# Performance work log

Hardware: AMD Instinct MI355X
Metric: run time of the kernel (lower is better)

Reference implementation:

```python
import jax, jax.numpy as jnp
import numpy as np

N = 50000
E = 800000
IN_DIM = 128
HID_DIM = 128
OUT_DIM = 128
EPS = 1e-5


def setup_inputs() -> dict:
    key = jax.random.key(0)
    ks = jax.random.split(key, 6)
    x = jax.random.normal(ks[0], (N, IN_DIM), dtype=jnp.float32)
    src = jax.random.randint(ks[1], (E,), 0, N, dtype=jnp.int32)
    dst = jax.random.randint(ks[2], (E,), 0, N, dtype=jnp.int32)
    W1 = jax.random.normal(ks[3], (IN_DIM, HID_DIM), dtype=jnp.float32) / np.sqrt(IN_DIM)
    W2 = jax.random.normal(ks[4], (HID_DIM, OUT_DIM), dtype=jnp.float32) / np.sqrt(HID_DIM)
    return {
        "x": x, "src": src, "dst": dst,
        "W1": W1, "b1": jnp.zeros((HID_DIM,), jnp.float32),
        "gamma1": jnp.ones((HID_DIM,), jnp.float32), "beta1": jnp.zeros((HID_DIM,), jnp.float32),
        "W2": W2, "b2": jnp.zeros((OUT_DIM,), jnp.float32),
        "gamma2": jnp.ones((OUT_DIM,), jnp.float32), "beta2": jnp.zeros((OUT_DIM,), jnp.float32),
    }


def _degrees(src, dst, n):
    ones = jnp.ones(src.shape[0], jnp.float32)
    out_deg = jax.ops.segment_sum(ones, src, num_segments=n)
    in_deg = jax.ops.segment_sum(ones, dst, num_segments=n)
    # DGL norm='both' clamps degree to min 1 before pow(-0.5)
    return jnp.clip(out_deg, 1.0) ** -0.5, jnp.clip(in_deg, 1.0) ** -0.5


def _gconv(h, src, dst, d_out, d_in, W, b):
    h = h * d_out[:, None]                                   # [N, d] src-side norm
    m = jax.ops.segment_sum(h[src], dst, num_segments=h.shape[0])  # SpMM aggregate
    m = m * d_in[:, None]                                    # dst-side norm
    return m @ W + b


def _bn(h, gamma, beta):
    mu = jnp.mean(h, axis=0)
    var = jnp.var(h, axis=0)  # biased, matches torch BN training forward
    return gamma * (h - mu) * jax.lax.rsqrt(var + EPS) + beta


def reference(x, src, dst, W1, b1, gamma1, beta1, W2, b2, gamma2, beta2):
    d_out, d_in = _degrees(src, dst, x.shape[0])
    h1 = jax.nn.relu(_bn(_gconv(x, src, dst, d_out, d_in, W1, b1), gamma1, beta1))
    # dropout is identity in eval mode
    h2 = _bn(_gconv(h1, src, dst, d_out, d_in, W2, b2), gamma2, beta2)
    return jax.nn.relu(h2 + h1)
```

## Files before the change

### kernel.cpp

```cpp
#include <hip/hip_runtime.h>
#include <hip/hip_fp16.h>

#define NODES 50000
#define EDGES 800000
#define DIM 128
#define EPS_BN 1e-5f
#define SCAN_B 1024
#define SCAN_NB ((NODES + SCAN_B - 1) / SCAN_B)
#define GEMM_NB ((NODES + 63) / 64)
#define NCH 64
#define CHE (EDGES / NCH)
#define NR 4
#define RNG (NODES / NR)

typedef _Float16 half8 __attribute__((ext_vector_type(8)));
typedef float floatx4 __attribute__((ext_vector_type(4)));

union H8 { half8 v; __half2 h2[4]; };

__global__ __launch_bounds__(256) void hist_part_kernel(const int* __restrict__ src,
                                                        const int* __restrict__ dst,
                                                        unsigned short* __restrict__ Psrc,
                                                        unsigned short* __restrict__ Pdst) {
    __shared__ int h[RNG];
    int chunk = blockIdx.x & (NCH - 1);
    int range = blockIdx.x >> 6;
    const int* arr = blockIdx.y ? dst : src;
    unsigned short* P = blockIdx.y ? Pdst : Psrc;
    int base = range * RNG;
    for (int i = threadIdx.x; i < RNG; i += 256) h[i] = 0;
    __syncthreads();
    int e0 = chunk * CHE;
    for (int e = e0 + threadIdx.x; e < e0 + CHE; e += 256) {
        unsigned r = (unsigned)(arr[e] - base);
        if (r < (unsigned)RNG) atomicAdd(&h[r], 1);
    }
    __syncthreads();
    for (int i = threadIdx.x; i < RNG; i += 256)
        P[(size_t)chunk * NODES + base + i] = (unsigned short)h[i];
}

__global__ __launch_bounds__(256) void combine_kernel(const unsigned short* __restrict__ Psrc,
                                                      unsigned short* __restrict__ Pdst,
                                                      int* __restrict__ cnt_in,
                                                      float* __restrict__ dn_out,
                                                      float* __restrict__ sdeg,
                                                      float* __restrict__ dn_in) {
    int v = blockIdx.x * 256 + threadIdx.x;
    if (v >= NODES) return;
    int s = 0;
    #pragma unroll 8
    for (int j = 0; j < NCH; ++j) s += Psrc[(size_t)j * NODES + v];
    float fs = (float)max(s, 1);
    dn_out[v] = rsqrtf(fs);
    sdeg[v] = sqrtf(fs);
    int run = 0;
    #pragma unroll 8
    for (int j = 0; j < NCH; ++j) {
        int t = Pdst[(size_t)j * NODES + v];
        Pdst[(size_t)j * NODES + v] = (unsigned short)run;
        run += t;
    }
    cnt_in[v] = run;
    dn_in[v] = rsqrtf((float)max(run, 1));
}

__global__ __launch_bounds__(SCAN_B) void scan_p1_kernel(const int* __restrict__ cnt,
                                                         int* __restrict__ row_ptr,
                                                         int* __restrict__ blk_sums) {
    __shared__ int sm[SCAN_B];
    int t = threadIdx.x;
    int idx = blockIdx.x * SCAN_B + t;
    int v = (idx < NODES) ? cnt[idx] : 0;
    sm[t] = v;
    __syncthreads();
    #pragma unroll
    for (int off = 1; off < SCAN_B; off <<= 1) {
        int u = (t >= off) ? sm[t - off] : 0;
        __syncthreads();
        sm[t] += u;
        __syncthreads();
    }
    if (idx < NODES) row_ptr[idx] = sm[t] - v;
    if (t == SCAN_B - 1) blk_sums[blockIdx.x] = sm[t];
}

__global__ __launch_bounds__(SCAN_B) void scan_p3_kernel(int* __restrict__ row_ptr,
                                                         const int* __restrict__ blk_sums) {
    __shared__ int soff;
    int t = threadIdx.x;
    if (t < 64) {
        int v = (t < blockIdx.x) ? blk_sums[t] : 0;
        #pragma unroll
        for (int off = 32; off > 0; off >>= 1) v += __shfl_xor(v, off);
        if (t == 0) soff = v;
    }
    __syncthreads();
    int idx = blockIdx.x * SCAN_B + t;
    if (idx < NODES) row_ptr[idx] += soff;
    if (idx == 0) row_ptr[NODES] = EDGES;
}

__global__ __launch_bounds__(256) void fill_kernel(const int* __restrict__ src,
                                                   const int* __restrict__ dst,
                                                   const int* __restrict__ row_ptr,
                                                   const unsigned short* __restrict__ Pdst,
                                                   int* __restrict__ csr_src) {
    __shared__ int h[RNG];
    int chunk = blockIdx.x & (NCH - 1);
    int range = blockIdx.x >> 6;
    int base = range * RNG;
    for (int i = threadIdx.x; i < RNG; i += 256) h[i] = 0;
    __syncthreads();
    int e0 = chunk * CHE;
    const unsigned short* Pj = Pdst + (size_t)chunk * NODES;
    for (int e = e0 + threadIdx.x; e < e0 + CHE; e += 256) {
        int d = dst[e];
        unsigned r = (unsigned)(d - base);
        if (r < (unsigned)RNG) {
            int local = atomicAdd(&h[r], 1);
            csr_src[row_ptr[d] + (int)Pj[d] + local] = src[e];
        }
    }
}

__global__ __launch_bounds__(256) void w2h_kernel(const float* __restrict__ W1,
                                                  const float* __restrict__ W2,
                                                  __half* __restrict__ WhT1,
                                                  __half* __restrict__ WhT2,
                                                  float* __restrict__ p2) {
    int idx = blockIdx.x * 256 + threadIdx.x;
    if (blockIdx.x < 32) p2[blockIdx.x * 256 + threadIdx.x] = 0.f;
    const float* W = (idx < 16384) ? W1 : W2;
    __half* D = (idx < 16384) ? WhT1 : WhT2;
    int i = idx & 16383;
    int n = i >> 7;
    int k = i & 127;
    D[i] = __float2half(W[k * DIM + n]);
}

__global__ __launch_bounds__(256) void prescale_kernel(const float* __restrict__ x,
                                                       const float* __restrict__ dn_out,
                                                       __half* __restrict__ hs) {
    int idx = blockIdx.x * 256 + threadIdx.x;
    if (idx >= NODES * 16) return;
    int row = idx >> 4;
    int c8 = (idx & 15) * 8;
    float sc = dn_out[row];
    const float* xp = x + (size_t)row * DIM + c8;
    float4 v0 = *(const float4*)xp;
    float4 v1 = *(const float4*)(xp + 4);
    H8 u;
    u.h2[0] = __floats2half2_rn(v0.x * sc, v0.y * sc);
    u.h2[1] = __floats2half2_rn(v0.z * sc, v0.w * sc);
    u.h2[2] = __floats2half2_rn(v1.x * sc, v1.y * sc);
    u.h2[3] = __floats2half2_rn(v1.z * sc, v1.w * sc);
    *(half8*)((char*)hs + ((size_t)row * DIM + c8) * 2) = u.v;
}

__device__ __forceinline__ void acc_h8(half8 raw, float* a) {
    H8 u; u.v = raw;
    #pragma unroll
    for (int k = 0; k < 4; ++k) {
        float2 f = __half22float2(u.h2[k]);
        a[2 * k] += f.x;
        a[2 * k + 1] += f.y;
    }
}

__global__ __launch_bounds__(256) void pull_kernel(const __half* __restrict__ hs,
                                                   const int* __restrict__ row_ptr,
                                                   const int* __restrict__ csr_src,
                                                   const float* __restrict__ dn_in,
                                                   __half* __restrict__ agg) {
    int wid = threadIdx.x >> 6;
    int node = blockIdx.x * 4 + wid;
    if (node >= NODES) return;
    int lane = threadIdx.x & 63;
    int q = lane >> 4;
    int c = lane & 15;
    const char* base = (const char*)hs;
    int beg = row_ptr[node];
    int end = row_ptr[node + 1];
    float a[8];
    #pragma unroll
    for (int i = 0; i < 8; ++i) a[i] = 0.f;
    int eb = beg;
    for (; eb + 8 <= end; eb += 8) {
        int s0 = csr_src[eb + q];
        int s1 = csr_src[eb + 4 + q];
        half8 v0 = *(const half8*)(base + (size_t)s0 * 256 + c * 16);
        half8 v1 = *(const half8*)(base + (size_t)s1 * 256 + c * 16);
        acc_h8(v0, a);
        acc_h8(v1, a);
    }
    for (; eb + 4 <= end; eb += 4) {
        int s0 = csr_src[eb + q];
        half8 v0 = *(const half8*)(base + (size_t)s0 * 256 + c * 16);
        acc_h8(v0, a);
    }
    if (eb + q < end) {
        int s0 = csr_src[eb + q];
        half8 v0 = *(const half8*)(base + (size_t)s0 * 256 + c * 16);
        acc_h8(v0, a);
    }
    #pragma unroll
    for (int i = 0; i < 8; ++i) a[i] += __shfl_xor(a[i], 32);
    #pragma unroll
    for (int i = 0; i < 8; ++i) a[i] += __shfl_xor(a[i], 16);
    if (lane < 16) {
        float sc = dn_in[node];
        H8 u;
        #pragma unroll
        for (int k = 0; k < 4; ++k)
            u.h2[k] = __floats2half2_rn(a[2 * k] * sc, a[2 * k + 1] * sc);
        *(half8*)((char*)agg + (size_t)node * 256 + c * 16) = u.v;
    }
}

__global__ __launch_bounds__(256) void gemm_mfma_kernel(const __half* __restrict__ A,
                                                        const __half* __restrict__ WhT,
                                                        const float* __restrict__ bias,
                                                        __half* __restrict__ hraw,
                                                        float* __restrict__ p2) {
    __shared__ float smem[8704];
    __half* wl = (__half*)smem;

    int t = threadIdx.x;

    #pragma unroll
    for (int i = 0; i < 8; ++i) {
        int cch = t + 256 * i;
        int n = cch >> 4;
        int ch = cch & 15;
        *(float4*)((char*)wl + n * 272 + ch * 16) =
            *(const float4*)((const char*)WhT + n * 256 + ch * 16);
    }

    int w = t >> 6;
    int lane = t & 63;
    int m = lane & 15;
    int quad = lane >> 4;
    int r0 = blockIdx.x * 64 + w * 16;
    int arow = r0 + m;

    half8 afrag[4];
    if (arow < NODES) {
        const char* ap = (const char*)(A + (size_t)arow * DIM);
        #pragma unroll
        for (int kt = 0; kt < 4; ++kt)
            afrag[kt] = *(const half8*)(ap + kt * 64 + quad * 16);
    } else {
        #pragma unroll
        for (int kt = 0; kt < 4; ++kt)
            #pragma unroll
            for (int j = 0; j < 8; ++j)
                afrag[kt][j] = (_Float16)0.0f;
    }

    floatx4 acc[8];
    floatx4 zf = {0.f, 0.f, 0.f, 0.f};
    #pragma unroll
    for (int ct = 0; ct < 8; ++ct) acc[ct] = zf;

    __syncthreads();

    #pragma unroll
    for (int kt = 0; kt < 4; ++kt) {
        #pragma unroll
        for (int ct = 0; ct < 8; ++ct) {
            half8 b = *(const half8*)((const char*)wl + (ct * 16 + m) * 272 + kt * 64 + quad * 16);
            acc[ct] = __builtin_amdgcn_mfma_f32_16x16x32_f16(afrag[kt], b, acc[ct], 0, 0, 0);
        }
    }

    __syncthreads();

    float* ps = smem;
    int g = w * 4 + quad;
    #pragma unroll
    for (int ct = 0; ct < 8; ++ct) {
        int col = ct * 16 + m;
        float bb = bias[col];
        float cs = 0.f, cq = 0.f;
        #pragma unroll
        for (int reg = 0; reg < 4; ++reg) {
            int row = r0 + quad * 4 + reg;
            if (row < NODES) {
                float o = acc[ct][reg] + bb;
                hraw[(size_t)row * DIM + col] = __float2half(o);
                cs += o;
                cq += o * o;
            }
        }
        ps[g * 128 + col] = cs;
        ps[2048 + g * 128 + col] = cq;
    }
    __syncthreads();

    float* pslot = p2 + (blockIdx.x & 31) * 256;
    if (t < 128) {
        float s = 0.f;
        #pragma unroll
        for (int gg = 0; gg < 16; ++gg) s += ps[gg * 128 + t];
        atomicAdd(pslot + t, s);
    } else {
        int cc = t - 128;
        float s = 0.f;
        #pragma unroll
        for (int gg = 0; gg < 16; ++gg) s += ps[2048 + gg * 128 + cc];
        atomicAdd(pslot + 128 + cc, s);
    }
}

__global__ __launch_bounds__(256) void stats_s2_kernel(float* __restrict__ p2,
                                                       float* __restrict__ stats) {
    int t = threadIdx.x;
    float s = 0.f;
    #pragma unroll
    for (int b = 0; b < 32; ++b) s += p2[b * 256 + t];
    stats[t] = s;
    #pragma unroll
    for (int b = 0; b < 32; ++b) p2[b * 256 + t] = 0.f;
}

__global__ __launch_bounds__(256) void bn_relu_scale_kernel(const __half* __restrict__ hraw,
                                                            __half* __restrict__ hs,
                                                            const float* __restrict__ stats,
                                                            const float* __restrict__ g,
                                                            const float* __restrict__ be,
                                                            const float* __restrict__ dn_out) {
    int idx = blockIdx.x * 256 + threadIdx.x;
    if (idx >= NODES * 16) return;
    int row = idx >> 4;
    int c8 = (idx & 15) * 8;
    const float invN = 1.0f / NODES;
    H8 u;
    u.v = *(const half8*)((const char*)hraw + ((size_t)row * DIM + c8) * 2);
    float o[8];
    #pragma unroll
    for (int k = 0; k < 4; ++k) {
        float2 f = __half22float2(u.h2[k]);
        o[2 * k] = f.x;
        o[2 * k + 1] = f.y;
    }
    #pragma unroll
    for (int j = 0; j < 8; ++j) {
        int cj = c8 + j;
        float mu = stats[cj] * invN;
        float var = stats[DIM + cj] * invN - mu * mu;
        float w = g[cj] * rsqrtf(var + EPS_BN);
        o[j] = fmaxf(w * (o[j] - mu) + be[cj], 0.f);
    }
    H8 us;
    float sc = dn_out[row];
    #pragma unroll
    for (int k = 0; k < 4; ++k)
        us.h2[k] = __floats2half2_rn(o[2 * k] * sc, o[2 * k + 1] * sc);
    *(half8*)((char*)hs + ((size_t)row * DIM + c8) * 2) = us.v;
}

__global__ __launch_bounds__(256) void bn_res_relu_kernel(const __half* __restrict__ hraw,
                                                          const __half* __restrict__ hs,
                                                          const float* __restrict__ sdeg,
                                                          float* __restrict__ out,
                                                          const float* __restrict__ stats,
                                                          const float* __restrict__ g,
                                                          const float* __restrict__ be) {
    int idx = blockIdx.x * 256 + threadIdx.x;
    if (idx >= NODES * 16) return;
    int row = idx >> 4;
    int c8 = (idx & 15) * 8;
    const float invN = 1.0f / NODES;
    float sd = sdeg[row];
    H8 u, ur;
    u.v = *(const half8*)((const char*)hraw + ((size_t)row * DIM + c8) * 2);
    ur.v = *(const half8*)((const char*)hs + ((size_t)row * DIM + c8) * 2);
    float o[8], r[8];
    #pragma unroll
    for (int k = 0; k < 4; ++k) {
        float2 f = __half22float2(u.h2[k]);
        float2 fr = __half22float2(ur.h2[k]);
        o[2 * k] = f.x; o[2 * k + 1] = f.y;
        r[2 * k] = fr.x * sd; r[2 * k + 1] = fr.y * sd;
    }
    #pragma unroll
    for (int j = 0; j < 8; ++j) {
        int cj = c8 + j;
        float mu = stats[cj] * invN;
        float var = stats[DIM + cj] * invN - mu * mu;
        float w = g[cj] * rsqrtf(var + EPS_BN);
        o[j] = fmaxf(w * (o[j] - mu) + be[cj] + r[j], 0.f);
    }
    float* op = out + (size_t)row * DIM + c8;
    float4 o0 = {o[0], o[1], o[2], o[3]};
    float4 o1 = {o[4], o[5], o[6], o[7]};
    *(float4*)op = o0;
    *(float4*)(op + 4) = o1;
}

extern "C" void kernel_launch(void* const* d_in, const int* in_sizes, int n_in,
                              void* d_out, int out_size, void* d_ws, size_t ws_size,
                              hipStream_t stream) {
    const float* x      = (const float*)d_in[0];
    const int*   src    = (const int*)d_in[1];
    const int*   dst    = (const int*)d_in[2];
    const float* W1     = (const float*)d_in[3];
    const float* b1     = (const float*)d_in[4];
    const float* gamma1 = (const float*)d_in[5];
    const float* beta1  = (const float*)d_in[6];
    const float* W2     = (const float*)d_in[7];
    const float* b2     = (const float*)d_in[8];
    const float* gamma2 = (const float*)d_in[9];
    const float* beta2  = (const float*)d_in[10];
    float* out = (float*)d_out;

    char* wsc = (char*)d_ws;
    int*   cnt_in   = (int*)wsc;                     wsc += NODES * 4;
    float* dn_out   = (float*)wsc;                   wsc += NODES * 4;
    float* sdeg     = (float*)wsc;                   wsc += NODES * 4;
    float* dn_in    = (float*)wsc;                   wsc += NODES * 4;
    int*   row_ptr  = (int*)wsc;                     wsc += (NODES + 1) * 4;
    int*   csr_src  = (int*)wsc;                     wsc += EDGES * 4;
    float* stats    = (float*)wsc;                   wsc += 2 * DIM * 4;
    int*   blk_sums = (int*)wsc;                     wsc += 64 * 4;
    __half* WhT1    = (__half*)wsc;                  wsc += DIM * DIM * 2;
    __half* WhT2    = (__half*)wsc;                  wsc += DIM * DIM * 2;
    float* p2       = (float*)wsc;                   wsc += 32 * 256 * 4;
    unsigned short* Psrc = (unsigned short*)wsc;     wsc += (size_t)NCH * NODES * 2;
    unsigned short* Pdst = (unsigned short*)wsc;     wsc += (size_t)NCH * NODES * 2;
    __half* hs      = (__half*)wsc;                  wsc += (size_t)NODES * DIM * 2;
    __half* agg     = (__half*)wsc;                  wsc += (size_t)NODES * DIM * 2;
    __half* hraw    = (__half*)wsc;                  wsc += (size_t)NODES * DIM * 2;

    const int T = 256;
    const int grid_pull = (NODES + 3) / 4;
    const int grid_e16  = (NODES * 16 + T - 1) / T;

    hist_part_kernel<<<dim3(NR * NCH, 2), T, 0, stream>>>(src, dst, Psrc, Pdst);
    combine_kernel<<<(NODES + T - 1) / T, T, 0, stream>>>(Psrc, Pdst, cnt_in, dn_out, sdeg, dn_in);
    scan_p1_kernel<<<SCAN_NB, SCAN_B, 0, stream>>>(cnt_in, row_ptr, blk_sums);
    scan_p3_kernel<<<SCAN_NB, SCAN_B, 0, stream>>>(row_ptr, blk_sums);
    fill_kernel<<<NR * NCH, T, 0, stream>>>(src, dst, row_ptr, Pdst, csr_src);

    w2h_kernel<<<128, T, 0, stream>>>(W1, W2, WhT1, WhT2, p2);

    prescale_kernel<<<grid_e16, T, 0, stream>>>(x, dn_out, hs);
    pull_kernel<<<grid_pull, T, 0, stream>>>(hs, row_ptr, csr_src, dn_in, agg);
    gemm_mfma_kernel<<<GEMM_NB, T, 0, stream>>>(agg, WhT1, b1, hraw, p2);
    stats_s2_kernel<<<1, T, 0, stream>>>(p2, stats);
    bn_relu_scale_kernel<<<grid_e16, T, 0, stream>>>(hraw, hs, stats, gamma1, beta1, dn_out);

    pull_kernel<<<grid_pull, T, 0, stream>>>(hs, row_ptr, csr_src, dn_in, agg);
    gemm_mfma_kernel<<<GEMM_NB, T, 0, stream>>>(agg, WhT2, b2, hraw, p2);
    stats_s2_kernel<<<1, T, 0, stream>>>(p2, stats);
    bn_res_relu_kernel<<<grid_e16, T, 0, stream>>>(hraw, hs, sdeg, out, stats, gamma2, beta2);
}
```

Before: 276.4 us.

## Bucket-sort edges by source before CSR build and use persistent pull waves

Adds a coarse 64-bucket counting sort of edges by source node ahead of the CSR construction. Each destination's neighbor list then comes out roughly ordered by source, which should improve gather locality in the pull kernels. The pull kernel also becomes grid-stride over a fixed 2048-block grid with an occupancy hint. The cost is three extra preprocessing kernels and two more edge-sized buffers of writes.

```diff
diff --git a/kernel.cpp b/kernel.cpp
--- a/kernel.cpp
+++ b/kernel.cpp
@@ -13,10 +13,72 @@
 #define NR 4
 #define RNG (NODES / NR)
 
+#define NBUK 64
+#define BUK_DIV 782
+#define SORT_NB 128
+#define EPB (EDGES / SORT_NB)
+
+#define PULL_NB 2048
+#define PULL_WAVES (PULL_NB * 4)
+
 typedef _Float16 half8 __attribute__((ext_vector_type(8)));
 typedef float floatx4 __attribute__((ext_vector_type(4)));
 
 union H8 { half8 v; __half2 h2[4]; };
+
+__global__ __launch_bounds__(256) void bucket_hist_kernel(const int* __restrict__ src,
+                                                          int* __restrict__ bins) {
+    __shared__ int lh[NBUK];
+    if (threadIdx.x < NBUK) lh[threadIdx.x] = 0;
+    __syncthreads();
+    int e0 = blockIdx.x * EPB;
+    for (int e = e0 + threadIdx.x; e < e0 + EPB; e += 256)
+        atomicAdd(&lh[src[e] / BUK_DIV], 1);
+    __syncthreads();
+    if (threadIdx.x < NBUK) atomicAdd(&bins[threadIdx.x], lh[threadIdx.x]);
+}
+
+__global__ void bucket_scan_kernel(const int* __restrict__ bins,
+                                   int* __restrict__ cursors) {
+    int t = threadIdx.x;
+    int v = bins[t];
+    int s = v;
+    #pragma unroll
+    for (int off = 1; off < 64; off <<= 1) {
+        int u = __shfl_up(s, off);
+        if (t >= off) s += u;
+    }
+    cursors[t] = s - v;
+}
+
+__global__ __launch_bounds__(256) void sort_scatter_kernel(const int* __restrict__ src,
+                                                           const int* __restrict__ dst,
+                                                           int* __restrict__ cursors,
+                                                           int* __restrict__ src2,
+                                                           int* __restrict__ dst2) {
+    __shared__ int lh[NBUK];
+    __shared__ int lbase[NBUK];
+    int t = threadIdx.x;
+    if (t < NBUK) lh[t] = 0;
+    __syncthreads();
+    int e0 = blockIdx.x * EPB;
+    for (int e = e0 + t; e < e0 + EPB; e += 256)
+        atomicAdd(&lh[src[e] / BUK_DIV], 1);
+    __syncthreads();
+    if (t < NBUK) {
+        lbase[t] = atomicAdd(&cursors[t], lh[t]);
+        lh[t] = 0;
+    }
+    __syncthreads();
+    for (int e = e0 + t; e < e0 + EPB; e += 256) {
+        int s = src[e];
+        int b = s / BUK_DIV;
+        int off = atomicAdd(&lh[b], 1);
+        int pos = lbase[b] + off;
+        src2[pos] = s;
+        dst2[pos] = dst[e];
+    }
+}
 
 __global__ __launch_bounds__(256) void hist_part_kernel(const int* __restrict__ src,
                                                         const int* __restrict__ dst,
@@ -128,9 +190,11 @@
                                                   const float* __restrict__ W2,
                                                   __half* __restrict__ WhT1,
                                                   __half* __restrict__ WhT2,
-                                                  float* __restrict__ p2) {
+                                                  float* __restrict__ p2,
+                                                  int* __restrict__ bins) {
     int idx = blockIdx.x * 256 + threadIdx.x;
     if (blockIdx.x < 32) p2[blockIdx.x * 256 + threadIdx.x] = 0.f;
+    if (blockIdx.x == 32 && threadIdx.x < NBUK) bins[threadIdx.x] = 0;
     const float* W = (idx < 16384) ? W1 : W2;
     __half* D = (idx < 16384) ? WhT1 : WhT2;
     int i = idx & 16383;
@@ -168,53 +232,54 @@
     }
 }
 
-__global__ __launch_bounds__(256) void pull_kernel(const __half* __restrict__ hs,
-                                                   const int* __restrict__ row_ptr,
-                                                   const int* __restrict__ csr_src,
-                                                   const float* __restrict__ dn_in,
-                                                   __half* __restrict__ agg) {
+__global__ __launch_bounds__(256, 8) void pull_kernel(const __half* __restrict__ hs,
+                                                      const int* __restrict__ row_ptr,
+                                                      const int* __restrict__ csr_src,
+                                                      const float* __restrict__ dn_in,
+                                                      __half* __restrict__ agg) {
     int wid = threadIdx.x >> 6;
-    int node = blockIdx.x * 4 + wid;
-    if (node >= NODES) return;
     int lane = threadIdx.x & 63;
     int q = lane >> 4;
     int c = lane & 15;
     const char* base = (const char*)hs;
-    int beg = row_ptr[node];
-    int end = row_ptr[node + 1];
-    float a[8];
-    #pragma unroll
-    for (int i = 0; i < 8; ++i) a[i] = 0.f;
-    int eb = beg;
-    for (; eb + 8 <= end; eb += 8) {
-        int s0 = csr_src[eb + q];
-        int s1 = csr_src[eb + 4 + q];
-        half8 v0 = *(const half8*)(base + (size_t)s0 * 256 + c * 16);
-        half8 v1 = *(const half8*)(base + (size_t)s1 * 256 + c * 16);
-        acc_h8(v0, a);
-        acc_h8(v1, a);
-    }
-    for (; eb + 4 <= end; eb += 4) {
-        int s0 = csr_src[eb + q];
-        half8 v0 = *(const half8*)(base + (size_t)s0 * 256 + c * 16);
-        acc_h8(v0, a);
-    }
-    if (eb + q < end) {
-        int s0 = csr_src[eb + q];
-        half8 v0 = *(const half8*)(base + (size_t)s0 * 256 + c * 16);
-        acc_h8(v0, a);
-    }
-    #pragma unroll
-    for (int i = 0; i < 8; ++i) a[i] += __shfl_xor(a[i], 32);
-    #pragma unroll
-    for (int i = 0; i < 8; ++i) a[i] += __shfl_xor(a[i], 16);
-    if (lane < 16) {
-        float sc = dn_in[node];
-        H8 u;
-        #pragma unroll
-        for (int k = 0; k < 4; ++k)
-            u.h2[k] = __floats2half2_rn(a[2 * k] * sc, a[2 * k + 1] * sc);
-        *(half8*)((char*)agg + (size_t)node * 256 + c * 16) = u.v;
+    int gw = blockIdx.x * 4 + wid;
+    for (int node = gw; node < NODES; node += PULL_WAVES) {
+        int beg = row_ptr[node];
+        int end = row_ptr[node + 1];
+        float a[8];
+        #pragma unroll
+        for (int i = 0; i < 8; ++i) a[i] = 0.f;
+        int eb = beg;
+        for (; eb + 8 <= end; eb += 8) {
+            int s0 = csr_src[eb + q];
+            int s1 = csr_src[eb + 4 + q];
+            half8 v0 = *(const half8*)(base + (size_t)s0 * 256 + c * 16);
+            half8 v1 = *(const half8*)(base + (size_t)s1 * 256 + c * 16);
+            acc_h8(v0, a);
+            acc_h8(v1, a);
+        }
+        for (; eb + 4 <= end; eb += 4) {
+            int s0 = csr_src[eb + q];
+            half8 v0 = *(const half8*)(base + (size_t)s0 * 256 + c * 16);
+            acc_h8(v0, a);
+        }
+        if (eb + q < end) {
+            int s0 = csr_src[eb + q];
+            half8 v0 = *(const half8*)(base + (size_t)s0 * 256 + c * 16);
+            acc_h8(v0, a);
+        }
+        #pragma unroll
+        for (int i = 0; i < 8; ++i) a[i] += __shfl_xor(a[i], 32);
+        #pragma unroll
+        for (int i = 0; i < 8; ++i) a[i] += __shfl_xor(a[i], 16);
+        if (lane < 16) {
+            float sc = dn_in[node];
+            H8 u;
+            #pragma unroll
+            for (int k = 0; k < 4; ++k)
+                u.h2[k] = __floats2half2_rn(a[2 * k] * sc, a[2 * k + 1] * sc);
+            *(half8*)((char*)agg + (size_t)node * 256 + c * 16) = u.v;
+        }
     }
 }
 
@@ -432,26 +497,33 @@
     __half* hs      = (__half*)wsc;                  wsc += (size_t)NODES * DIM * 2;
     __half* agg     = (__half*)wsc;                  wsc += (size_t)NODES * DIM * 2;
     __half* hraw    = (__half*)wsc;                  wsc += (size_t)NODES * DIM * 2;
+    int*   src2     = (int*)wsc;                     wsc += EDGES * 4;
+    int*   dst2     = (int*)wsc;                     wsc += EDGES * 4;
+    int*   bins     = (int*)wsc;                     wsc += NBUK * 4;
+    int*   cursors  = (int*)wsc;                     wsc += NBUK * 4;
 
     const int T = 256;
-    const int grid_pull = (NODES + 3) / 4;
     const int grid_e16  = (NODES * 16 + T - 1) / T;
 
-    hist_part_kernel<<<dim3(NR * NCH, 2), T, 0, stream>>>(src, dst, Psrc, Pdst);
+    w2h_kernel<<<128, T, 0, stream>>>(W1, W2, WhT1, WhT2, p2, bins);
+
+    bucket_hist_kernel<<<SORT_NB, T, 0, stream>>>(src, bins);
+    bucket_scan_kernel<<<1, 64, 0, stream>>>(bins, cursors);
+    sort_scatter_kernel<<<SORT_NB, T, 0, stream>>>(src, dst, cursors, src2, dst2);
+
+    hist_part_kernel<<<dim3(NR * NCH, 2), T, 0, stream>>>(src2, dst2, Psrc, Pdst);
     combine_kernel<<<(NODES + T - 1) / T, T, 0, stream>>>(Psrc, Pdst, cnt_in, dn_out, sdeg, dn_in);
     scan_p1_kernel<<<SCAN_NB, SCAN_B, 0, stream>>>(cnt_in, row_ptr, blk_sums);
     scan_p3_kernel<<<SCAN_NB, SCAN_B, 0, stream>>>(row_ptr, blk_sums);
-    fill_kernel<<<NR * NCH, T, 0, stream>>>(src, dst, row_ptr, Pdst, csr_src);
-
-    w2h_kernel<<<128, T, 0, stream>>>(W1, W2, WhT1, WhT2, p2);
+    fill_kernel<<<NR * NCH, T, 0, stream>>>(src2, dst2, row_ptr, Pdst, csr_src);
 
     prescale_kernel<<<grid_e16, T, 0, stream>>>(x, dn_out, hs);
-    pull_kernel<<<grid_pull, T, 0, stream>>>(hs, row_ptr, csr_src, dn_in, agg);
+    pull_kernel<<<PULL_NB, T, 0, stream>>>(hs, row_ptr, csr_src, dn_in, agg);
     gemm_mfma_kernel<<<GEMM_NB, T, 0, stream>>>(agg, WhT1, b1, hraw, p2);
     stats_s2_kernel<<<1, T, 0, stream>>>(p2, stats);
     bn_relu_scale_kernel<<<grid_e16, T, 0, stream>>>(hraw, hs, stats, gamma1, beta1, dn_out);
 
-    pull_kernel<<<grid_pull, T, 0, stream>>>(hs, row_ptr, csr_src, dn_in, agg);
+    pull_kernel<<<PULL_NB, T, 0, stream>>>(hs, row_ptr, csr_src, dn_in, agg);
     gemm_mfma_kernel<<<GEMM_NB, T, 0, stream>>>(agg, WhT2, b2, hraw, p2);
     stats_s2_kernel<<<1, T, 0, stream>>>(p2, stats);
     bn_res_relu_kernel<<<grid_e16, T, 0, stream>>>(hraw, hs, sdeg, out, stats, gamma2, beta2);
```

Result: slower. 310.0 us (+12.2%).
